# Performance work log

Hardware: AMD Instinct MI355X
Metric: run time of the kernel (lower is better)

## Reference

```python
import jax, jax.numpy as jnp
import numpy as np

D_MODEL = 1024
N_HEADS = 16
D_HEAD = D_MODEL // N_HEADS  # 64
D_FF = D_MODEL  # FeedForward(d_model, d_model) in source
B, S = 4, 1024
EPS = 1e-5


def layer_norm(x, gamma, beta):
    mu = jnp.mean(x, axis=-1, keepdims=True)
    var = jnp.mean(jnp.square(x - mu), axis=-1, keepdims=True)
    return (x - mu) * jax.lax.rsqrt(var + EPS) * gamma + beta


def setup_inputs() -> dict:
    key = jax.random.key(0)
    ks = jax.random.split(key, 16)
    s_embed = 1.0 / np.sqrt(D_MODEL)
    s_ff = 1.0 / np.sqrt(D_FF)
    return {
        "x": jax.random.normal(ks[0], (B, S, D_MODEL), jnp.float32),
        # per-head QKV projections stacked over heads: [H, d_embed, d_head]
        "Wq": jax.random.normal(ks[1], (N_HEADS, D_MODEL, D_HEAD), jnp.float32) * s_embed,
        "bq": jax.random.normal(ks[2], (N_HEADS, D_HEAD), jnp.float32) * s_embed,
        "Wk": jax.random.normal(ks[3], (N_HEADS, D_MODEL, D_HEAD), jnp.float32) * s_embed,
        "bk": jax.random.normal(ks[4], (N_HEADS, D_HEAD), jnp.float32) * s_embed,
        "Wv": jax.random.normal(ks[5], (N_HEADS, D_MODEL, D_HEAD), jnp.float32) * s_embed,
        "bv": jax.random.normal(ks[6], (N_HEADS, D_HEAD), jnp.float32) * s_embed,
        "Wo": jax.random.normal(ks[7], (D_MODEL, D_MODEL), jnp.float32) * s_embed,
        "bo": jax.random.normal(ks[8], (D_MODEL,), jnp.float32) * s_embed,
        "g1": jnp.ones((D_MODEL,), jnp.float32),
        "be1": jnp.zeros((D_MODEL,), jnp.float32),
        "W1": jax.random.normal(ks[9], (D_MODEL, D_FF), jnp.float32) * s_embed,
        "b1": jax.random.normal(ks[10], (D_FF,), jnp.float32) * s_embed,
        "W2": jax.random.normal(ks[11], (D_FF, D_MODEL), jnp.float32) * s_ff,
        "b2": jax.random.normal(ks[12], (D_MODEL,), jnp.float32) * s_ff,
        "g2": jnp.ones((D_MODEL,), jnp.float32),
        "be2": jnp.zeros((D_MODEL,), jnp.float32),
    }


def reference(x, Wq, bq, Wk, bk, Wv, bv, Wo, bo, g1, be1, W1, b1, W2, b2, g2, be2):
    scale = 1.0 / np.sqrt(D_HEAD).astype(np.float32)
    # batched per-head projections (equivalent to the per-head Linear loop)
    Q = jnp.einsum('bse,hed->bhsd', x, Wq) + bq[None, :, None, :]
    K = jnp.einsum('bse,hed->bhsd', x, Wk) + bk[None, :, None, :]
    V = jnp.einsum('bse,hed->bhsd', x, Wv) + bv[None, :, None, :]
    scores = jnp.einsum('bhsd,bhtd->bhst', Q, K) * scale
    attn = jax.nn.softmax(scores, axis=-1)
    ctx = jnp.einsum('bhst,bhtd->bhsd', attn, V)
    # concat heads along feature dim (head order matches the torch cat)
    ctx = jnp.transpose(ctx, (0, 2, 1, 3)).reshape(x.shape[0], x.shape[1], D_MODEL)
    attn_out = ctx @ Wo + bo
    y1 = layer_norm(x + attn_out, g1, be1)
    ff = jax.nn.relu(y1 @ W1 + b1) @ W2 + b2  # dropout is identity in eval
    return layer_norm(y1 + ff, g2, be2)
```

## Files before the change

kernel.cpp:

```cpp
#include <hip/hip_runtime.h>
#include <stdint.h>

#define BSZ 4
#define SEQ 1024
#define DM 1024
#define NH 16
#define DH 64
#define ROWS (BSZ * SEQ)
#define QS3 3072

typedef unsigned short u16;
typedef short bf16x8 __attribute__((ext_vector_type(8)));
typedef float f32x4 __attribute__((ext_vector_type(4)));

__device__ __forceinline__ float b2f(u16 u) {
    union { uint32_t i; float f; } v; v.i = ((uint32_t)u) << 16; return v.f;
}
__device__ __forceinline__ u16 f2b(float f) {
    union { float f; uint32_t i; } v; v.f = f;
    uint32_t u = v.i;
    return (u16)((u + 0x7FFFu + ((u >> 16) & 1u)) >> 16);
}
__device__ __forceinline__ u16 f2b_rh(float f) {
    union { float f; uint32_t i; } v; v.f = f;
    return (u16)((v.i + 0x8000u) >> 16);
}

__device__ __forceinline__ size_t blk_idx(int row, int col, int nkt) {
    return (((size_t)((row >> 7) * nkt + (col >> 5))) << 12)
         + ((((row >> 4) & 7) * 64 + ((col >> 3) & 3) * 16 + (row & 15)) << 3)
         + (col & 7);
}

typedef const __attribute__((address_space(1))) void gv_t;
typedef __attribute__((address_space(3))) void lv_t;
__device__ __forceinline__ void gl_lds16(const void* g, void* l) {
    __builtin_amdgcn_global_load_lds((gv_t*)g, (lv_t*)l, 16, 0, 0);
}

__device__ __forceinline__ int detect_isf(const uint32_t* __restrict__ x) {
    const int lane = threadIdx.x & 63;
    const uint4 wv = *(const uint4*)(x + lane * 4);
    uint32_t ws[4] = {wv.x, wv.y, wv.z, wv.w};
    int c = 0;
    #pragma unroll
    for (int j = 0; j < 4; ++j) {
        uint32_t lo = ws[j] & 0xFFFFu;
        uint32_t e = (lo >> 7) & 0xFF;
        if ((e >= 100 && e <= 140) || lo == 0) c++;
    }
    #pragma unroll
    for (int d = 1; d < 64; d <<= 1) c += __shfl_xor(c, d);
    return c < 128;
}

__global__ __launch_bounds__(256) void prep_all(
    const void* x_raw, const void* Wq, const void* Wk, const void* Wv,
    const void* Wo, const void* W1, const void* W2,
    const void* bq, const void* bk, const void* bv, const void* bo,
    const void* b1, const void* b2, const void* g1, const void* be1,
    const void* g2, const void* be2,
    u16* __restrict__ x_b, u16* __restrict__ WqkvB, u16* __restrict__ WoB,
    u16* __restrict__ W1B, u16* __restrict__ W2B, u16* __restrict__ vecs)
{
    const int bid = blockIdx.x, tid = threadIdx.x;
    const int isf = detect_isf((const uint32_t*)x_raw);

    if (bid < 2048) {
        const int gid = bid * 256 + tid;
        const int tile = gid >> 9, c = gid & 511;
        const int p = tile >> 5, t = tile & 31;
        const int r = p * 128 + ((c >> 6) & 7) * 16 + (c & 15);
        const int k = t * 32 + ((c >> 4) & 3) * 8;
        union { uint4 q; u16 s[8]; } o;
        if (isf) {
            const float* s = (const float*)x_raw + (size_t)r * DM + k;
            float4 f0 = *(const float4*)s;
            float4 f1 = *(const float4*)(s + 4);
            o.s[0] = f2b(f0.x); o.s[1] = f2b(f0.y); o.s[2] = f2b(f0.z); o.s[3] = f2b(f0.w);
            o.s[4] = f2b(f1.x); o.s[5] = f2b(f1.y); o.s[6] = f2b(f1.z); o.s[7] = f2b(f1.w);
        } else {
            o.q = *(const uint4*)((const u16*)x_raw + (size_t)r * DM + k);
        }
        *(uint4*)&x_b[(size_t)gid * 8] = o.q;
        return;
    }
    if (bid >= 8192) {
        const int i = (bid - 8192) * 256 + tid;
        const int seg = i >> 10, off = i & 1023;
        const void* srcs[10] = {bq, bk, bv, bo, b1, b2, g1, be1, g2, be2};
        const void* s = srcs[seg];
        vecs[i] = isf ? f2b(((const float*)s)[off]) : ((const u16*)s)[off];
        return;
    }

    const void* src; u16* dst; int R, C, n_off, bx, by, z;
    if (bid < 5120) {
        const int which = (bid - 2048) >> 10;
        const int lb = (bid - 2048) & 1023;
        src = which == 0 ? Wq : (which == 1 ? Wk : Wv);
        dst = WqkvB; R = DM; C = DH; n_off = which * 1024;
        bx = lb & 1; by = (lb >> 1) & 31; z = lb >> 6;
    } else {
        const int which = (bid - 5120) >> 10;
        const int lb = (bid - 5120) & 1023;
        src = which == 0 ? Wo : (which == 1 ? W1 : W2);
        dst = which == 0 ? WoB : (which == 1 ? W1B : W2B);
        R = DM; C = DM; n_off = 0;
        bx = lb & 31; by = (lb >> 5) & 31; z = 0;
    }

    __shared__ u16 Ts[32][33];
    const int cb = bx * 32, rb = by * 32;
    const int tr = tid >> 3, tc4 = (tid & 7) * 4;
    const size_t sbase = (size_t)z * R * C;

    u16 v[4];
    if (isf) {
        const float* s = (const float*)src + sbase + (size_t)(rb + tr) * C + cb + tc4;
        float4 f = *(const float4*)s;
        v[0] = f2b(f.x); v[1] = f2b(f.y); v[2] = f2b(f.z); v[3] = f2b(f.w);
    } else {
        const u16* s = (const u16*)src + sbase + (size_t)(rb + tr) * C + cb + tc4;
        ushort4 f = *(const ushort4*)s;
        v[0] = f.x; v[1] = f.y; v[2] = f.z; v[3] = f.w;
    }
    #pragma unroll
    for (int j = 0; j < 4; ++j) Ts[tc4 + j][tr] = v[j];
    __syncthreads();

    if (tid < 128) {
        const int np = tid & 31, qp = tid >> 5;
        const int n = n_off + z * C + cb + np;
        const int k = rb + qp * 8;
        union { uint4 q; u16 s[8]; } o;
        #pragma unroll
        for (int j = 0; j < 8; ++j) o.s[j] = Ts[np][qp * 8 + j];
        *(uint4*)&dst[blk_idx(n, k, 32)] = o.q;
    }
}

__global__ __launch_bounds__(256) void gemm_qkv(
    const u16* __restrict__ Ab, const u16* __restrict__ Bb,
    const u16* __restrict__ bias,
    u16* __restrict__ Qblk, u16* __restrict__ Kblk, u16* __restrict__ Vblk)
{
    __shared__ uint4 smem4[3072];
    u16* As = (u16*)smem4;
    u16* Bs = (u16*)smem4 + 12288;
    u16* Cs = (u16*)smem4;

    const int tid = threadIdx.x;
    const int w = tid >> 6, lane = tid & 63;
    const int l16 = lane & 15, quad = lane >> 4;
    const int wr = w >> 1, wc = w & 1;
    const int bm = blockIdx.y * 128, bn = blockIdx.x * 128;
    const int nkt = 32;

    const u16* At = Ab + ((size_t)(bm >> 7) * nkt << 12);
    const u16* Bt = Bb + ((size_t)(bn >> 7) * nkt << 12);

    f32x4 acc[4][4];
    #pragma unroll
    for (int i = 0; i < 4; ++i)
        #pragma unroll
        for (int j = 0; j < 4; ++j)
            acc[i][j] = (f32x4){0.f, 0.f, 0.f, 0.f};

#define STAGE_QKV(t, bf) do {                                              \
        const size_t tb_ = (size_t)(t) << 12;                              \
        gl_lds16(&At[tb_ + (w * 64 + lane) * 8],       As + (bf) * 4096 + w * 512);        \
        gl_lds16(&At[tb_ + (256 + w * 64 + lane) * 8], As + (bf) * 4096 + 2048 + w * 512); \
        gl_lds16(&Bt[tb_ + (w * 64 + lane) * 8],       Bs + (bf) * 4096 + w * 512);        \
        gl_lds16(&Bt[tb_ + (256 + w * 64 + lane) * 8], Bs + (bf) * 4096 + 2048 + w * 512); \
    } while (0)

    STAGE_QKV(0, 0);
    STAGE_QKV(1, 1);
    asm volatile("s_waitcnt vmcnt(4)" ::: "memory");
    __builtin_amdgcn_s_barrier();

    int cur = 0, nb = 2;
    for (int kt = 0; kt < nkt; ++kt) {
        if (kt + 2 < nkt) STAGE_QKV(kt + 2, nb);

        bf16x8 a[4], b[4];
        #pragma unroll
        for (int i = 0; i < 4; ++i)
            a[i] = *(const bf16x8*)&As[cur * 4096 + (((wr * 4 + i) * 64) + quad * 16 + l16) * 8];
        #pragma unroll
        for (int j = 0; j < 4; ++j)
            b[j] = *(const bf16x8*)&Bs[cur * 4096 + (((wc * 4 + j) * 64) + quad * 16 + l16) * 8];

        #pragma unroll
        for (int i = 0; i < 4; ++i)
            #pragma unroll
            for (int j = 0; j < 4; ++j)
                acc[i][j] = __builtin_amdgcn_mfma_f32_16x16x32_bf16(a[i], b[j], acc[i][j], 0, 0, 0);

        if (kt + 2 < nkt) {
            asm volatile("s_waitcnt vmcnt(4)" ::: "memory");
            __builtin_amdgcn_s_barrier();
        } else if (kt + 1 < nkt) {
            asm volatile("s_waitcnt vmcnt(0)" ::: "memory");
            __builtin_amdgcn_s_barrier();
        }
        cur = cur == 2 ? 0 : cur + 1;
        nb  = nb  == 2 ? 0 : nb + 1;
    }
    __syncthreads();
#undef STAGE_QKV

    #pragma unroll
    for (int j = 0; j < 4; ++j) {
        const int lc = wc * 64 + j * 16 + l16;
        const float bj = b2f(bias[bn + lc]);
        #pragma unroll
        for (int i = 0; i < 4; ++i)
            #pragma unroll
            for (int r = 0; r < 4; ++r) {
                const int lr = wr * 64 + i * 16 + quad * 4 + r;
                Cs[lr * 136 + lc] = f2b(acc[i][j][r] + bj);
            }
    }
    __syncthreads();

    const int b_ = bm >> 10, sb16 = (bm & 1023) >> 4, kb64 = (bm & 1023) >> 6;
    if (bn < 2048) {
        u16* out = (bn < 1024) ? Qblk : Kblk;
        const int hbase = (bn & 1023) >> 6;
        #pragma unroll
        for (int u = 0; u < 8; ++u) {
            const int g = u * 256 + tid;
            const int hh = g >> 10, rem = g & 1023;
            const int s16r = rem >> 7, rem2 = rem & 127;
            const int half = rem2 >> 6, lam = rem2 & 63;
            const int row = s16r * 16 + (lam & 15);
            const int col = hh * 64 + half * 32 + (lam >> 4) * 8;
            uint4 val = *(const uint4*)&Cs[row * 136 + col];
            const size_t gi = ((size_t)((b_ * 16 + hbase + hh) * 64 + sb16 + s16r)) * 1024
                            + half * 512 + (size_t)lam * 8;
            *(uint4*)&out[gi] = val;
        }
    } else {
        const int hbase = (bn - 2048) >> 6;
        #pragma unroll
        for (int u = 0; u < 8; ++u) {
            const int g = u * 256 + tid;
            const int hh = g >> 10, rem = g & 1023;
            const int kt64r = rem >> 9, dt = (rem >> 7) & 3;
            const int half = (rem >> 6) & 1, lam = rem & 63;
            const int d = dt * 16 + (lam & 15);
            const int s0 = kt64r * 64 + half * 32 + (lam >> 4) * 8;
            union { uint4 q; u16 s[8]; } o;
            #pragma unroll
            for (int j = 0; j < 8; ++j) o.s[j] = Cs[(s0 + j) * 136 + hh * 64 + d];
            const size_t gi = ((size_t)((b_ * 16 + hbase + hh) * 16 + kb64 + kt64r)) * 4096
                            + dt * 1024 + half * 512 + (size_t)lam * 8;
            *(uint4*)&Vblk[gi] = o.q;
        }
    }
}

__global__ __launch_bounds__(512) void attn_mfma(
    const u16* __restrict__ Qblk, const u16* __restrict__ Kblk,
    const u16* __restrict__ Vblk, u16* __restrict__ ctx)
{
    __shared__ u16 Qf[8192];
    __shared__ u16 Kf[2][4096];
    __shared__ u16 Vf[2][4096];
    __shared__ u16 Ps[8 * 16 * 72];

    const int qt = blockIdx.x, h = blockIdx.y, b = blockIdx.z;
    const int tid = threadIdx.x;
    const int w = tid >> 6, lane = tid & 63;
    const int l16 = lane & 15, quad = lane >> 4;
    const size_t qrow0 = (size_t)(b * SEQ + qt * 128);
    const int bh = b * NH + h;
    const int hoff = h * DH;

    const u16* Qg = Qblk + ((size_t)(bh * 64 + qt * 8 + w)) * 1024 + (size_t)lane * 8;
    gl_lds16(Qg,       &Qf[w * 1024]);
    gl_lds16(Qg + 512, &Qf[w * 1024 + 512]);

    const u16* Kg = Kblk + ((size_t)(bh * 64)) * 1024 + (size_t)w * 512 + (size_t)lane * 8;
    const u16* Vg = Vblk + ((size_t)(bh * 16)) * 4096 + (size_t)w * 512 + (size_t)lane * 8;

    gl_lds16(Kg, &Kf[0][w * 512]);
    gl_lds16(Vg, &Vf[0][w * 512]);
    __syncthreads();

    bf16x8 aQ0 = *(const bf16x8*)&Qf[w * 1024 +       lane * 8];
    bf16x8 aQ1 = *(const bf16x8*)&Qf[w * 1024 + 512 + lane * 8];

    f32x4 O[4];
    #pragma unroll
    for (int dt = 0; dt < 4; ++dt) O[dt] = (f32x4){0.f, 0.f, 0.f, 0.f};
    float lacc[4] = {0.f, 0.f, 0.f, 0.f};

    for (int kt64 = 0; kt64 < SEQ / 64; ++kt64) {
        const int cur = kt64 & 1, nxt = cur ^ 1;
        if (kt64 + 1 < SEQ / 64) {
            gl_lds16(Kg + (size_t)(kt64 + 1) * 4096, &Kf[nxt][w * 512]);
            gl_lds16(Vg + (size_t)(kt64 + 1) * 4096, &Vf[nxt][w * 512]);
        }

        f32x4 St[4];
        #pragma unroll
        for (int t = 0; t < 4; ++t) {
            bf16x8 b0 = *(const bf16x8*)&Kf[cur][t * 1024 +       lane * 8];
            bf16x8 b1 = *(const bf16x8*)&Kf[cur][t * 1024 + 512 + lane * 8];
            f32x4 z = (f32x4){0.f, 0.f, 0.f, 0.f};
            z = __builtin_amdgcn_mfma_f32_16x16x32_bf16(aQ0, b0, z, 0, 0, 0);
            z = __builtin_amdgcn_mfma_f32_16x16x32_bf16(aQ1, b1, z, 0, 0, 0);
            St[t] = z;
        }

        #pragma unroll
        for (int t = 0; t < 4; ++t)
            #pragma unroll
            for (int r = 0; r < 4; ++r) {
                const float p = __expf(St[t][r] * 0.125f);
                lacc[r] += p;
                Ps[w * 1152 + (quad * 4 + r) * 72 + t * 16 + l16] = f2b_rh(p);
            }

        bf16x8 aP0 = *(const bf16x8*)&Ps[w * 1152 + l16 * 72 +  0 + quad * 8];
        bf16x8 aP1 = *(const bf16x8*)&Ps[w * 1152 + l16 * 72 + 32 + quad * 8];
        #pragma unroll
        for (int dt = 0; dt < 4; ++dt) {
            bf16x8 vv0 = *(const bf16x8*)&Vf[cur][dt * 1024 +       lane * 8];
            bf16x8 vv1 = *(const bf16x8*)&Vf[cur][dt * 1024 + 512 + lane * 8];
            O[dt] = __builtin_amdgcn_mfma_f32_16x16x32_bf16(aP0, vv0, O[dt], 0, 0, 0);
            O[dt] = __builtin_amdgcn_mfma_f32_16x16x32_bf16(aP1, vv1, O[dt], 0, 0, 0);
        }
        __syncthreads();
    }

    const size_t pbase = ((size_t)(qrow0 >> 7) * 32) << 12;
    #pragma unroll
    for (int r = 0; r < 4; ++r) {
        float s = lacc[r];
        s += __shfl_xor(s, 1);
        s += __shfl_xor(s, 2);
        s += __shfl_xor(s, 4);
        s += __shfl_xor(s, 8);
        const float inv = 1.0f / s;
        #pragma unroll
        for (int dt = 0; dt < 4; ++dt) {
            const int t = (hoff + dt * 16) >> 5;
            const int q = (((hoff + dt * 16) >> 3) & 3);
            const size_t idx = pbase + ((size_t)t << 12)
                             + ((w * 64 + q * 16 + quad * 4 + r) << 3) + (l16 & 7);
            const size_t idx2 = idx + (((size_t)(l16 >> 3)) << 7);
            ctx[idx2] = f2b(O[dt][r] * inv);
        }
    }
}

__global__ __launch_bounds__(256) void gemm_b64(
    const u16* __restrict__ Ab, const u16* __restrict__ Bb,
    const u16* __restrict__ bias, const u16* __restrict__ resid,
    u16* __restrict__ C, int N,
    int relu, int c_blocked, int resid_blocked)
{
    __shared__ uint4 smem4[2304];
    u16* As = (u16*)smem4;
    u16* Bs = (u16*)smem4 + 12288;
    u16* Cs = (u16*)smem4;

    const int tid = threadIdx.x;
    const int w = tid >> 6, lane = tid & 63;
    const int l16 = lane & 15, quad = lane >> 4;
    const int bm = blockIdx.y * 128, bn = blockIdx.x * 64;
    const int nkt = 32;

    const u16* At = Ab + ((size_t)(bm >> 7) * nkt << 12);
    const int bsub = ((bn >> 6) & 1) * 256;
    const u16* Bt = Bb + ((size_t)(bn >> 7) * nkt << 12);

    f32x4 acc[2][4];
    #pragma unroll
    for (int i = 0; i < 2; ++i)
        #pragma unroll
        for (int j = 0; j < 4; ++j)
            acc[i][j] = (f32x4){0.f, 0.f, 0.f, 0.f};

#define STAGE_B64(t, bf) do {                                              \
        const size_t tb_ = (size_t)(t) << 12;                              \
        gl_lds16(&At[tb_ + (w * 64 + lane) * 8],        As + (bf) * 4096 + w * 512);        \
        gl_lds16(&At[tb_ + (256 + w * 64 + lane) * 8],  As + (bf) * 4096 + 2048 + w * 512); \
        gl_lds16(&Bt[tb_ + (bsub + w * 64 + lane) * 8], Bs + (bf) * 2048 + w * 512);        \
    } while (0)

    STAGE_B64(0, 0);
    STAGE_B64(1, 1);
    asm volatile("s_waitcnt vmcnt(3)" ::: "memory");
    __builtin_amdgcn_s_barrier();

    int cur = 0, nb = 2;
    for (int kt = 0; kt < nkt; ++kt) {
        if (kt + 2 < nkt) STAGE_B64(kt + 2, nb);

        bf16x8 a[2], b[4];
        #pragma unroll
        for (int i = 0; i < 2; ++i)
            a[i] = *(const bf16x8*)&As[cur * 4096 + (((w * 2 + i) * 64) + quad * 16 + l16) * 8];
        #pragma unroll
        for (int j = 0; j < 4; ++j)
            b[j] = *(const bf16x8*)&Bs[cur * 2048 + ((j * 64) + quad * 16 + l16) * 8];

        #pragma unroll
        for (int i = 0; i < 2; ++i)
            #pragma unroll
            for (int j = 0; j < 4; ++j)
                acc[i][j] = __builtin_amdgcn_mfma_f32_16x16x32_bf16(a[i], b[j], acc[i][j], 0, 0, 0);

        if (kt + 2 < nkt) {
            asm volatile("s_waitcnt vmcnt(3)" ::: "memory");
            __builtin_amdgcn_s_barrier();
        } else if (kt + 1 < nkt) {
            asm volatile("s_waitcnt vmcnt(0)" ::: "memory");
            __builtin_amdgcn_s_barrier();
        }
        cur = cur == 2 ? 0 : cur + 1;
        nb  = nb  == 2 ? 0 : nb + 1;
    }
    __syncthreads();
#undef STAGE_B64

    #pragma unroll
    for (int j = 0; j < 4; ++j) {
        const int lc = j * 16 + l16;
        const int col = bn + lc;
        const float bj = bias ? b2f(bias[col]) : 0.f;
        #pragma unroll
        for (int i = 0; i < 2; ++i) {
            #pragma unroll
            for (int r = 0; r < 4; ++r) {
                const int lr = w * 32 + i * 16 + quad * 4 + r;
                float v = acc[i][j][r] + bj;
                if (resid) {
                    const size_t ri = resid_blocked ? blk_idx(bm + lr, col, N >> 5)
                                                    : (size_t)(bm + lr) * N + col;
                    v += b2f(resid[ri]);
                }
                if (relu) v = v > 0.f ? v : 0.f;
                Cs[lr * 72 + lc] = f2b(v);
            }
        }
    }
    __syncthreads();

    if (!c_blocked) {
        #pragma unroll
        for (int u = 0; u < 4; ++u) {
            const int g = u * 256 + tid;
            const int row = g >> 3, c16 = g & 7;
            uint4 val = *(const uint4*)&Cs[row * 72 + c16 * 8];
            *(uint4*)&C[(size_t)(bm + row) * N + bn + c16 * 8] = val;
        }
    } else {
        const size_t obase = ((size_t)((bm >> 7) * (N >> 5) + (bn >> 5))) << 12;
        #pragma unroll
        for (int u = 0; u < 4; ++u) {
            const int cc = u * 256 + tid;
            const int t2 = cc >> 9, c = cc & 511;
            const int row = ((c >> 6) & 7) * 16 + (c & 15);
            const int col = t2 * 32 + ((c >> 4) & 3) * 8;
            uint4 val = *(const uint4*)&Cs[row * 72 + col];
            *(uint4*)&C[obase + ((size_t)t2 << 12) + (size_t)c * 8] = val;
        }
    }
}

__device__ __forceinline__ void ln8(
    const u16* __restrict__ X, const u16* __restrict__ gamma,
    const u16* __restrict__ beta, void* __restrict__ Y,
    int y_mode, int isf, int row0)
{
    const int tid = threadIdx.x;
    const int w = tid >> 6, lane = tid & 63;
    union U8 { uint4 q; u16 h[8]; };

    U8 ga, gb, ba, bb;
    ga.q = *(const uint4*)(gamma + lane * 16);
    gb.q = *(const uint4*)(gamma + lane * 16 + 8);
    ba.q = *(const uint4*)(beta  + lane * 16);
    bb.q = *(const uint4*)(beta  + lane * 16 + 8);
    float g[16], be[16];
    #pragma unroll
    for (int j = 0; j < 8; ++j) {
        g[j] = b2f(ga.h[j]);  g[8 + j] = b2f(gb.h[j]);
        be[j] = b2f(ba.h[j]); be[8 + j] = b2f(bb.h[j]);
    }

    #pragma unroll
    for (int it = 0; it < 2; ++it) {
        const int r = row0 + it * 4 + w;
        const u16* xp = X + (size_t)r * DM + lane * 16;
        U8 xa, xb;
        xa.q = *(const uint4*)xp;
        xb.q = *(const uint4*)(xp + 8);
        float xv[16], s = 0.f, s2 = 0.f;
        #pragma unroll
        for (int j = 0; j < 8; ++j) { xv[j] = b2f(xa.h[j]); xv[8 + j] = b2f(xb.h[j]); }
        #pragma unroll
        for (int j = 0; j < 16; ++j) { s += xv[j]; s2 += xv[j] * xv[j]; }
        #pragma unroll
        for (int d = 1; d < 64; d <<= 1) {
            s  += __shfl_xor(s, d);
            s2 += __shfl_xor(s2, d);
        }
        const float mu = s * (1.0f / DM);
        const float rstd = rsqrtf(s2 * (1.0f / DM) - mu * mu + 1e-5f);

        float y[16];
        #pragma unroll
        for (int j = 0; j < 16; ++j) y[j] = (xv[j] - mu) * rstd * g[j] + be[j];

        if (y_mode == 1) {
            #pragma unroll
            for (int c = 0; c < 2; ++c) {
                U8 o;
                #pragma unroll
                for (int j = 0; j < 8; ++j) o.h[j] = f2b(y[c * 8 + j]);
                *(uint4*)&((u16*)Y)[blk_idx(r, lane * 16 + c * 8, 32)] = o.q;
            }
        } else {
            if (isf) {
                float* yp = (float*)Y + (size_t)r * DM + lane * 16;
                #pragma unroll
                for (int c = 0; c < 4; ++c) {
                    float4 f; f.x = y[c*4]; f.y = y[c*4+1]; f.z = y[c*4+2]; f.w = y[c*4+3];
                    *(float4*)(yp + c * 4) = f;
                }
            } else {
                u16* yp = (u16*)Y + (size_t)r * DM + lane * 16;
                #pragma unroll
                for (int c = 0; c < 2; ++c) {
                    U8 o;
                    #pragma unroll
                    for (int j = 0; j < 8; ++j) o.h[j] = f2b(y[c * 8 + j]);
                    *(uint4*)(yp + c * 8) = o.q;
                }
            }
        }
    }
}

__global__ __launch_bounds__(256) void layernorm8(
    const u16* __restrict__ X, const u16* __restrict__ gamma,
    const u16* __restrict__ beta, void* __restrict__ Y,
    const uint32_t* __restrict__ xraw, int y_mode)
{
    const int isf = (y_mode == 2) ? detect_isf(xraw) : 0;
    ln8(X, gamma, beta, Y, y_mode, isf, blockIdx.x * 8);
}

extern "C" void kernel_launch(void* const* d_in, const int* in_sizes, int n_in,
                              void* d_out, int out_size, void* d_ws, size_t ws_size,
                              hipStream_t stream) {
    const void* x_raw   = d_in[0];
    const void* Wq_raw  = d_in[1];
    const void* bq_raw  = d_in[2];
    const void* Wk_raw  = d_in[3];
    const void* bk_raw  = d_in[4];
    const void* Wv_raw  = d_in[5];
    const void* bv_raw  = d_in[6];
    const void* Wo_raw  = d_in[7];
    const void* bo_raw  = d_in[8];
    const void* g1_raw  = d_in[9];
    const void* be1_raw = d_in[10];
    const void* W1_raw  = d_in[11];
    const void* b1_raw  = d_in[12];
    const void* W2_raw  = d_in[13];
    const void* b2_raw  = d_in[14];
    const void* g2_raw  = d_in[15];
    const void* be2_raw = d_in[16];

    char* ws = (char*)d_ws;
    const size_t MB = 1024 * 1024;
    u16* x_b    = (u16*)(ws + 1 * MB);
    u16* WqkvB  = (u16*)(ws + 9 * MB);
    u16* WoB    = (u16*)(ws + 15 * MB);
    u16* W1B    = (u16*)(ws + 17 * MB);
    u16* W2B    = (u16*)(ws + 19 * MB);
    u16* vecs   = (u16*)(ws + 21 * MB);
    u16* bqkv_c = vecs;
    u16* bo_c   = vecs + 3072;
    u16* b1_c   = vecs + 4096;
    u16* b2_c   = vecs + 5120;
    u16* g1_c   = vecs + 6144;
    u16* be1_c  = vecs + 7168;
    u16* g2_c   = vecs + 8192;
    u16* be2_c  = vecs + 9216;
    u16* Qblk   = (u16*)(ws + 22 * MB);
    u16* Kblk   = (u16*)(ws + 30 * MB);
    u16* Vblk   = (u16*)(ws + 38 * MB);
    u16* ctxB   = (u16*)(ws + 48 * MB);
    u16* res1   = (u16*)(ws + 56 * MB);
    u16* y1B    = Qblk;
    u16* hmidB  = Kblk;
    u16* res2   = res1;

    prep_all<<<8232, 256, 0, stream>>>(
        x_raw, Wq_raw, Wk_raw, Wv_raw, Wo_raw, W1_raw, W2_raw,
        bq_raw, bk_raw, bv_raw, bo_raw, b1_raw, b2_raw,
        g1_raw, be1_raw, g2_raw, be2_raw,
        x_b, WqkvB, WoB, W1B, W2B, vecs);

    gemm_qkv<<<dim3(QS3 / 128, ROWS / 128), 256, 0, stream>>>(
        x_b, WqkvB, bqkv_c, Qblk, Kblk, Vblk);

    attn_mfma<<<dim3(SEQ / 128, NH, BSZ), 512, 0, stream>>>(Qblk, Kblk, Vblk, ctxB);

    dim3 gg64(DM / 64, ROWS / 128);
    gemm_b64<<<gg64, 256, 0, stream>>>(ctxB, WoB, bo_c, x_b, res1, DM, 0, 0, 1);
    layernorm8<<<ROWS / 8, 256, 0, stream>>>(res1, g1_c, be1_c, (void*)y1B, nullptr, 1);
    gemm_b64<<<gg64, 256, 0, stream>>>(y1B, W1B, b1_c, nullptr, hmidB, DM, 1, 1, 0);
    gemm_b64<<<gg64, 256, 0, stream>>>(hmidB, W2B, b2_c, y1B, res2, DM, 0, 0, 1);
    layernorm8<<<ROWS / 8, 256, 0, stream>>>(res2, g2_c, be2_c, d_out,
                                             (const uint32_t*)x_raw, 2);
}
```

Measured before the change: 253.7 us.

## Use 128x128 tiles for dense GEMMs and XCD-aware block remapping across kernels

Result: slower. 270.1 us (+6.5%).

```diff
diff --git a/kernel.cpp b/kernel.cpp
--- a/kernel.cpp
+++ b/kernel.cpp
@@ -154,7 +154,12 @@
     const int w = tid >> 6, lane = tid & 63;
     const int l16 = lane & 15, quad = lane >> 4;
     const int wr = w >> 1, wc = w & 1;
-    const int bm = blockIdx.y * 128, bn = blockIdx.x * 128;
+
+    const int fid = blockIdx.x;
+    const int xcd = fid & 7, t = fid >> 3;
+    const int byi = ((xcd & 3) << 3) + (t & 7);
+    const int bxi = (xcd >> 2) * 12 + (t >> 3);
+    const int bm = byi * 128, bn = bxi * 128;
     const int nkt = 32;
 
     const u16* At = Ab + ((size_t)(bm >> 7) * nkt << 12);
@@ -167,22 +172,22 @@
         for (int j = 0; j < 4; ++j)
             acc[i][j] = (f32x4){0.f, 0.f, 0.f, 0.f};
 
-#define STAGE_QKV(t, bf) do {                                              \
-        const size_t tb_ = (size_t)(t) << 12;                              \
+#define STAGE_T(t_, bf) do {                                               \
+        const size_t tb_ = (size_t)(t_) << 12;                             \
         gl_lds16(&At[tb_ + (w * 64 + lane) * 8],       As + (bf) * 4096 + w * 512);        \
         gl_lds16(&At[tb_ + (256 + w * 64 + lane) * 8], As + (bf) * 4096 + 2048 + w * 512); \
         gl_lds16(&Bt[tb_ + (w * 64 + lane) * 8],       Bs + (bf) * 4096 + w * 512);        \
         gl_lds16(&Bt[tb_ + (256 + w * 64 + lane) * 8], Bs + (bf) * 4096 + 2048 + w * 512); \
     } while (0)
 
-    STAGE_QKV(0, 0);
-    STAGE_QKV(1, 1);
+    STAGE_T(0, 0);
+    STAGE_T(1, 1);
     asm volatile("s_waitcnt vmcnt(4)" ::: "memory");
     __builtin_amdgcn_s_barrier();
 
     int cur = 0, nb = 2;
     for (int kt = 0; kt < nkt; ++kt) {
-        if (kt + 2 < nkt) STAGE_QKV(kt + 2, nb);
+        if (kt + 2 < nkt) STAGE_T(kt + 2, nb);
 
         bf16x8 a[4], b[4];
         #pragma unroll
@@ -209,7 +214,7 @@
         nb  = nb  == 2 ? 0 : nb + 1;
     }
     __syncthreads();
-#undef STAGE_QKV
+#undef STAGE_T
 
     #pragma unroll
     for (int j = 0; j < 4; ++j) {
@@ -271,12 +276,16 @@
     __shared__ u16 Vf[2][4096];
     __shared__ u16 Ps[8 * 16 * 72];
 
-    const int qt = blockIdx.x, h = blockIdx.y, b = blockIdx.z;
+    const int fid = blockIdx.x;
+    const int xcd = fid & 7, tt = fid >> 3;
+    const int bh = (xcd << 3) + (tt >> 3);
+    const int qt = tt & 7;
+    const int b = bh >> 4, h = bh & 15;
+
     const int tid = threadIdx.x;
     const int w = tid >> 6, lane = tid & 63;
     const int l16 = lane & 15, quad = lane >> 4;
     const size_t qrow0 = (size_t)(b * SEQ + qt * 128);
-    const int bh = b * NH + h;
     const int hoff = h * DH;
 
     const u16* Qg = Qblk + ((size_t)(bh * 64 + qt * 8 + w)) * 1024 + (size_t)lane * 8;
@@ -358,13 +367,13 @@
     }
 }
 
-__global__ __launch_bounds__(256) void gemm_b64(
+__global__ __launch_bounds__(256) void gemm_b128(
     const u16* __restrict__ Ab, const u16* __restrict__ Bb,
     const u16* __restrict__ bias, const u16* __restrict__ resid,
-    u16* __restrict__ C, int N,
+    u16* __restrict__ C,
     int relu, int c_blocked, int resid_blocked)
 {
-    __shared__ uint4 smem4[2304];
+    __shared__ uint4 smem4[3072];
     u16* As = (u16*)smem4;
     u16* Bs = (u16*)smem4 + 12288;
     u16* Cs = (u16*)smem4;
@@ -372,52 +381,58 @@
     const int tid = threadIdx.x;
     const int w = tid >> 6, lane = tid & 63;
     const int l16 = lane & 15, quad = lane >> 4;
-    const int bm = blockIdx.y * 128, bn = blockIdx.x * 64;
+    const int wr = w >> 1, wc = w & 1;
+
+    const int fid = blockIdx.x;
+    const int xcd = fid & 7, t = fid >> 3;
+    const int byi = ((xcd & 3) << 3) + (t & 7);
+    const int bxi = ((xcd >> 2) << 2) + (t >> 3);
+    const int bm = byi * 128, bn = bxi * 128;
     const int nkt = 32;
 
     const u16* At = Ab + ((size_t)(bm >> 7) * nkt << 12);
-    const int bsub = ((bn >> 6) & 1) * 256;
     const u16* Bt = Bb + ((size_t)(bn >> 7) * nkt << 12);
 
-    f32x4 acc[2][4];
-    #pragma unroll
-    for (int i = 0; i < 2; ++i)
+    f32x4 acc[4][4];
+    #pragma unroll
+    for (int i = 0; i < 4; ++i)
         #pragma unroll
         for (int j = 0; j < 4; ++j)
             acc[i][j] = (f32x4){0.f, 0.f, 0.f, 0.f};
 
-#define STAGE_B64(t, bf) do {                                              \
-        const size_t tb_ = (size_t)(t) << 12;                              \
-        gl_lds16(&At[tb_ + (w * 64 + lane) * 8],        As + (bf) * 4096 + w * 512);        \
-        gl_lds16(&At[tb_ + (256 + w * 64 + lane) * 8],  As + (bf) * 4096 + 2048 + w * 512); \
-        gl_lds16(&Bt[tb_ + (bsub + w * 64 + lane) * 8], Bs + (bf) * 2048 + w * 512);        \
+#define STAGE_T(t_, bf) do {                                               \
+        const size_t tb_ = (size_t)(t_) << 12;                             \
+        gl_lds16(&At[tb_ + (w * 64 + lane) * 8],       As + (bf) * 4096 + w * 512);        \
+        gl_lds16(&At[tb_ + (256 + w * 64 + lane) * 8], As + (bf) * 4096 + 2048 + w * 512); \
+        gl_lds16(&Bt[tb_ + (w * 64 + lane) * 8],       Bs + (bf) * 4096 + w * 512);        \
+        gl_lds16(&Bt[tb_ + (256 + w * 64 + lane) * 8], Bs + (bf) * 4096 + 2048 + w * 512); \
     } while (0)
 
-    STAGE_B64(0, 0);
-    STAGE_B64(1, 1);
-    asm volatile("s_waitcnt vmcnt(3)" ::: "memory");
+    STAGE_T(0, 0);
+    STAGE_T(1, 1);
+    asm volatile("s_waitcnt vmcnt(4)" ::: "memory");
     __builtin_amdgcn_s_barrier();
 
     int cur = 0, nb = 2;
     for (int kt = 0; kt < nkt; ++kt) {
-        if (kt + 2 < nkt) STAGE_B64(kt + 2, nb);
-
-        bf16x8 a[2], b[4];
-        #pragma unroll
-        for (int i = 0; i < 2; ++i)
-            a[i] = *(const bf16x8*)&As[cur * 4096 + (((w * 2 + i) * 64) + quad * 16 + l16) * 8];
+        if (kt + 2 < nkt) STAGE_T(kt + 2, nb);
+
+        bf16x8 a[4], b[4];
+        #pragma unroll
+        for (int i = 0; i < 4; ++i)
+            a[i] = *(const bf16x8*)&As[cur * 4096 + (((wr * 4 + i) * 64) + quad * 16 + l16) * 8];
         #pragma unroll
         for (int j = 0; j < 4; ++j)
-            b[j] = *(const bf16x8*)&Bs[cur * 2048 + ((j * 64) + quad * 16 + l16) * 8];
-
-        #pragma unroll
-        for (int i = 0; i < 2; ++i)
+            b[j] = *(const bf16x8*)&Bs[cur * 4096 + (((wc * 4 + j) * 64) + quad * 16 + l16) * 8];
+
+        #pragma unroll
+        for (int i = 0; i < 4; ++i)
             #pragma unroll
             for (int j = 0; j < 4; ++j)
                 acc[i][j] = __builtin_amdgcn_mfma_f32_16x16x32_bf16(a[i], b[j], acc[i][j], 0, 0, 0);
 
         if (kt + 2 < nkt) {
-            asm volatile("s_waitcnt vmcnt(3)" ::: "memory");
+            asm volatile("s_waitcnt vmcnt(4)" ::: "memory");
             __builtin_amdgcn_s_barrier();
         } else if (kt + 1 < nkt) {
             asm volatile("s_waitcnt vmcnt(0)" ::: "memory");
@@ -427,26 +442,26 @@
         nb  = nb  == 2 ? 0 : nb + 1;
     }
     __syncthreads();
-#undef STAGE_B64
+#undef STAGE_T
 
     #pragma unroll
     for (int j = 0; j < 4; ++j) {
-        const int lc = j * 16 + l16;
+        const int lc = wc * 64 + j * 16 + l16;
         const int col = bn + lc;
         const float bj = bias ? b2f(bias[col]) : 0.f;
         #pragma unroll
-        for (int i = 0; i < 2; ++i) {
+        for (int i = 0; i < 4; ++i) {
             #pragma unroll
             for (int r = 0; r < 4; ++r) {
-                const int lr = w * 32 + i * 16 + quad * 4 + r;
+                const int lr = wr * 64 + i * 16 + quad * 4 + r;
                 float v = acc[i][j][r] + bj;
                 if (resid) {
-                    const size_t ri = resid_blocked ? blk_idx(bm + lr, col, N >> 5)
-                                                    : (size_t)(bm + lr) * N + col;
+                    const size_t ri = resid_blocked ? blk_idx(bm + lr, col, 32)
+                                                    : (size_t)(bm + lr) * DM + col;
                     v += b2f(resid[ri]);
                 }
                 if (relu) v = v > 0.f ? v : 0.f;
-                Cs[lr * 72 + lc] = f2b(v);
+                Cs[lr * 136 + lc] = f2b(v);
             }
         }
     }
@@ -454,21 +469,21 @@
 
     if (!c_blocked) {
         #pragma unroll
-        for (int u = 0; u < 4; ++u) {
+        for (int u = 0; u < 8; ++u) {
             const int g = u * 256 + tid;
-            const int row = g >> 3, c16 = g & 7;
-            uint4 val = *(const uint4*)&Cs[row * 72 + c16 * 8];
-            *(uint4*)&C[(size_t)(bm + row) * N + bn + c16 * 8] = val;
+            const int row = g >> 4, c16 = g & 15;
+            uint4 val = *(const uint4*)&Cs[row * 136 + c16 * 8];
+            *(uint4*)&C[(size_t)(bm + row) * DM + bn + c16 * 8] = val;
         }
     } else {
-        const size_t obase = ((size_t)((bm >> 7) * (N >> 5) + (bn >> 5))) << 12;
-        #pragma unroll
-        for (int u = 0; u < 4; ++u) {
+        const size_t obase = ((size_t)((bm >> 7) * 32 + (bn >> 5))) << 12;
+        #pragma unroll
+        for (int u = 0; u < 8; ++u) {
             const int cc = u * 256 + tid;
             const int t2 = cc >> 9, c = cc & 511;
             const int row = ((c >> 6) & 7) * 16 + (c & 15);
             const int col = t2 * 32 + ((c >> 4) & 3) * 8;
-            uint4 val = *(const uint4*)&Cs[row * 72 + col];
+            uint4 val = *(const uint4*)&Cs[row * 136 + col];
             *(uint4*)&C[obase + ((size_t)t2 << 12) + (size_t)c * 8] = val;
         }
     }
@@ -610,16 +625,14 @@
         g1_raw, be1_raw, g2_raw, be2_raw,
         x_b, WqkvB, WoB, W1B, W2B, vecs);
 
-    gemm_qkv<<<dim3(QS3 / 128, ROWS / 128), 256, 0, stream>>>(
-        x_b, WqkvB, bqkv_c, Qblk, Kblk, Vblk);
-
-    attn_mfma<<<dim3(SEQ / 128, NH, BSZ), 512, 0, stream>>>(Qblk, Kblk, Vblk, ctxB);
-
-    dim3 gg64(DM / 64, ROWS / 128);
-    gemm_b64<<<gg64, 256, 0, stream>>>(ctxB, WoB, bo_c, x_b, res1, DM, 0, 0, 1);
+    gemm_qkv<<<768, 256, 0, stream>>>(x_b, WqkvB, bqkv_c, Qblk, Kblk, Vblk);
+
+    attn_mfma<<<512, 256 * 2, 0, stream>>>(Qblk, Kblk, Vblk, ctxB);
+
+    gemm_b128<<<256, 256, 0, stream>>>(ctxB, WoB, bo_c, x_b, res1, 0, 0, 1);
     layernorm8<<<ROWS / 8, 256, 0, stream>>>(res1, g1_c, be1_c, (void*)y1B, nullptr, 1);
-    gemm_b64<<<gg64, 256, 0, stream>>>(y1B, W1B, b1_c, nullptr, hmidB, DM, 1, 1, 0);
-    gemm_b64<<<gg64, 256, 0, stream>>>(hmidB, W2B, b2_c, y1B, res2, DM, 0, 0, 1);
+    gemm_b128<<<256, 256, 0, stream>>>(y1B, W1B, b1_c, nullptr, hmidB, 1, 1, 0);
+    gemm_b128<<<256, 256, 0, stream>>>(hmidB, W2B, b2_c, y1B, res2, 0, 0, 1);
     layernorm8<<<ROWS / 8, 256, 0, stream>>>(res2, g2_c, be2_c, d_out,
                                              (const uint32_t*)x_raw, 2);
 }
```
